# Optimization experiments

Hardware: AMD Instinct MI355X
Metric: run time of the kernel (lower is better)

The kernel has to match this reference:

```python
import jax, jax.numpy as jnp
import numpy as np

SCOPE = 63          # length of ricker inhibition filter (odd)
IN_CHANNELS = 256   # circulant matrix size == channel dim
SELF_CONNECT = False


def ricker(scope, width, damp, self_connect=False):
    # symmetric ricker (mexican-hat) wavelet of length `scope`, centered
    x = jnp.arange(scope, dtype=jnp.float32) - scope // 2
    w2 = width * width
    r = damp * (1.0 - x * x / w2) * jnp.exp(-x * x / (2.0 * w2))
    if not self_connect:
        r = r.at[scope // 2].set(0.0)  # no self-connection: zero center tap
    return r


def toeplitz1d_circular(f, size):
    # embed the centered length-`scope` filter into the first row of a
    # size x size circulant matrix (center tap on the diagonal, tails wrap)
    half = f.shape[0] // 2
    row0 = jnp.zeros(size, f.dtype)
    row0 = row0.at[: half + 1].set(f[half:])      # center + right tail
    row0 = row0.at[size - half:].set(f[:half])    # left tail wraps around
    idx = (jnp.arange(size)[:, None] - jnp.arange(size)[None, :]) % size
    return row0[idx]  # C[i, j] = row0[(i - j) mod size]


def setup_inputs() -> dict:
    key = jax.random.key(0)
    activations = jax.random.normal(key, (64, IN_CHANNELS, 56, 56), dtype=jnp.float32)
    damp = jnp.asarray(0.12, dtype=jnp.float32)   # learnable scalar
    width = jnp.asarray(3.0, dtype=jnp.float32)   # learnable scalar
    return {"activations": activations, "damp": damp, "width": width}


def reference(activations, damp, width):
    f = ricker(SCOPE, width, damp, SELF_CONNECT)
    tpl = toeplitz1d_circular(f, IN_CHANNELS)
    tpl_inv = jnp.linalg.inv(jnp.eye(IN_CHANNELS, dtype=f.dtype) - tpl)
    # apply inhibition matrix along the channel axis at every pixel
    return jnp.einsum('ij,bjhw->bihw', tpl_inv, activations)
```

## Files before the change

kernel.cpp:

```cpp
#include <hip/hip_runtime.h>


#define IN_CH 256
#define HW    3136
#define TP    64

typedef _Float16 f16x8  __attribute__((ext_vector_type(8)));
typedef float    f32x16 __attribute__((ext_vector_type(16)));


__global__ __launch_bounds__(256) void pi_build(const float* __restrict__ damp,
                                                const float* __restrict__ width,
                                                f16x8* __restrict__ afrag) {
    __shared__ float cS[256], gS[256], ctab[256], mS[256];
    int t = threadIdx.x;
    float w = width[0], dmp = damp[0];

    ctab[t] = cosf((float)t * 0.0245436926f );

    int x = (t < 128) ? t : t - 256;
    float cv = 0.0f;
    if (t != 0 && x >= -31 && x <= 31) {
        float fx2 = (float)(x * x);
        float w2  = w * w;
        cv = dmp * (1.0f - fx2 / w2) * expf(-fx2 / (2.0f * w2));
    }
    cS[t] = cv;
    __syncthreads();

    float lam = 0.0f;
#pragma unroll 8
    for (int n = 0; n < 256; n++) lam += cS[n] * ctab[(t * n) & 255];
    gS[t] = 1.0f / (1.0f - lam);
    __syncthreads();

    float md = 0.0f;
#pragma unroll 8
    for (int k = 0; k < 256; k++) md += gS[k] * ctab[(t * k) & 255];
    mS[t] = md * (1.0f / 256.0f);
    __syncthreads();

#pragma unroll
    for (int g = 0; g < 32; g++) {
        int gid = g * 256 + t;
        int l  = gid & 63;
        int tt = (gid >> 6) & 7;
        int s  = gid >> 9;
        int i     = 32 * tt + (l & 31);
        int kbase = 16 * s + 8 * (l >> 5);
        f16x8 h;
#pragma unroll
        for (int j = 0; j < 8; j++)
            h[j] = (_Float16)mS[(i - (kbase + j)) & 255];
        afrag[gid] = h;
    }
}

__device__ __forceinline__ void loads16(const float* __restrict__ src, float* v) {
#pragma unroll
    for (int j = 0; j < 8; j++) {
        v[j]     = src[(size_t)j * HW];
        v[8 + j] = src[(size_t)j * HW + 32];
    }
}

__device__ __forceinline__ void compute16(const float* v,
                                          const f16x8* __restrict__ afrag,
                                          int base, int lane,
                                          f32x16 acc[2][2]) {
    f16x8 b0, b1;
#pragma unroll
    for (int j = 0; j < 8; j++) {
        b0[j] = (_Float16)v[j];
        b1[j] = (_Float16)v[8 + j];
    }
    f16x8 a0 = afrag[(base + 0) * 64 + lane];
    f16x8 a1 = afrag[(base + 1) * 64 + lane];
    acc[0][0] = __builtin_amdgcn_mfma_f32_32x32x16_f16(a0, b0, acc[0][0], 0, 0, 0);
    acc[0][1] = __builtin_amdgcn_mfma_f32_32x32x16_f16(a0, b1, acc[0][1], 0, 0, 0);
    acc[1][0] = __builtin_amdgcn_mfma_f32_32x32x16_f16(a1, b0, acc[1][0], 0, 0, 0);
    acc[1][1] = __builtin_amdgcn_mfma_f32_32x32x16_f16(a1, b1, acc[1][1], 0, 0, 0);
}

__global__ __launch_bounds__(256, 4) void pi_gemm(const float* __restrict__ act,
                                                  float* __restrict__ out,
                                                  const f16x8* __restrict__ afrag) {
    int tid  = threadIdx.x;
    int lane = tid & 63;
    int wv   = tid >> 6;

    int b    = blockIdx.x / 49;
    int tile = blockIdx.x - b * 49;
    int p0   = tile * TP;

    int col   = lane & 31;
    int khalf = (lane >> 5) * 8;

    const float* actb = act + (size_t)b * (IN_CH * HW) + p0 + col;
    float*       outb = out + (size_t)b * (IN_CH * HW) + p0 + col;

    f32x16 acc[2][2] = {};

    float v0[16], v1[16];
    const float* ksrc = actb + (size_t)khalf * HW;

    loads16(ksrc, v0);
#pragma unroll
    for (int ss = 0; ss < 8; ss++) {
        loads16(ksrc + (size_t)(16 * (2 * ss + 1)) * HW, v1);
        compute16(v0, afrag, (2 * ss) * 8 + 2 * wv, lane, acc);
        if (ss < 7)
            loads16(ksrc + (size_t)(16 * (2 * ss + 2)) * HW, v0);
        compute16(v1, afrag, (2 * ss + 1) * 8 + 2 * wv, lane, acc);
    }

    int rb = 4 * (lane >> 5);
#pragma unroll
    for (int ti = 0; ti < 2; ti++) {
#pragma unroll
        for (int ni = 0; ni < 2; ni++) {
            float* dst = outb + (size_t)(64 * wv + 32 * ti + rb) * HW + 32 * ni;
#pragma unroll
            for (int r = 0; r < 16; r++) {
                int row = (r & 3) + 8 * (r >> 2);
                __builtin_nontemporal_store(acc[ti][ni][r], dst + (size_t)row * HW);
            }
        }
    }
}

extern "C" void kernel_launch(void* const* d_in, const int* in_sizes, int n_in,
                              void* d_out, int out_size, void* d_ws, size_t ws_size,
                              hipStream_t stream) {
    const float* act   = (const float*)d_in[0];
    const float* damp  = (const float*)d_in[1];
    const float* width = (const float*)d_in[2];
    float* out = (float*)d_out;

    f16x8* afrag = (f16x8*)d_ws;
    int batches = in_sizes[0] / (IN_CH * HW);

    pi_build<<<1, 256, 0, stream>>>(damp, width, afrag);
    pi_gemm<<<batches * 49, 256, 0, stream>>>(act, out, afrag);
}
```

Before: 383.3 us.

## Stage activation tiles through LDS with async global_load_lds pipeline

Replaces per-lane strided register loads of the activation tile with 16-byte global_load_lds transfers into a 4-deep LDS ring buffer, shared across the four waves. Each wave now loads only a quarter of the K slice and reads B fragments from LDS, with explicit vmcnt waits and barriers pipelining three stages ahead. This is meant to cut redundant global traffic, since each wave previously reloaded the full activation slice, and to widen the memory requests. In exchange it adds 32KB of LDS per block, which may limit occupancy at 4 blocks per CU, plus block-wide barriers.

```diff
diff --git a/kernel.cpp b/kernel.cpp
--- a/kernel.cpp
+++ b/kernel.cpp
@@ -4,9 +4,11 @@
 #define IN_CH 256
 #define HW    3136
 #define TP    64
+#define KS    32
 
 typedef _Float16 f16x8  __attribute__((ext_vector_type(8)));
 typedef float    f32x16 __attribute__((ext_vector_type(16)));
+typedef unsigned int u32;
 
 
 __global__ __launch_bounds__(256) void pi_build(const float* __restrict__ damp,
@@ -56,35 +58,17 @@
     }
 }
 
-__device__ __forceinline__ void loads16(const float* __restrict__ src, float* v) {
-#pragma unroll
-    for (int j = 0; j < 8; j++) {
-        v[j]     = src[(size_t)j * HW];
-        v[8 + j] = src[(size_t)j * HW + 32];
-    }
-}
-
-__device__ __forceinline__ void compute16(const float* v,
-                                          const f16x8* __restrict__ afrag,
-                                          int base, int lane,
-                                          f32x16 acc[2][2]) {
-    f16x8 b0, b1;
-#pragma unroll
-    for (int j = 0; j < 8; j++) {
-        b0[j] = (_Float16)v[j];
-        b1[j] = (_Float16)v[8 + j];
-    }
-    f16x8 a0 = afrag[(base + 0) * 64 + lane];
-    f16x8 a1 = afrag[(base + 1) * 64 + lane];
-    acc[0][0] = __builtin_amdgcn_mfma_f32_32x32x16_f16(a0, b0, acc[0][0], 0, 0, 0);
-    acc[0][1] = __builtin_amdgcn_mfma_f32_32x32x16_f16(a0, b1, acc[0][1], 0, 0, 0);
-    acc[1][0] = __builtin_amdgcn_mfma_f32_32x32x16_f16(a1, b0, acc[1][0], 0, 0, 0);
-    acc[1][1] = __builtin_amdgcn_mfma_f32_32x32x16_f16(a1, b1, acc[1][1], 0, 0, 0);
+__device__ __forceinline__ void gl_lds16(const float* g, const float* l) {
+    __builtin_amdgcn_global_load_lds(
+        (const __attribute__((address_space(1))) u32*)g,
+        (__attribute__((address_space(3))) u32*)l, 16, 0, 0);
 }
 
 __global__ __launch_bounds__(256, 4) void pi_gemm(const float* __restrict__ act,
                                                   float* __restrict__ out,
                                                   const f16x8* __restrict__ afrag) {
+    __shared__ float lds[4][KS][TP];
+
     int tid  = threadIdx.x;
     int lane = tid & 63;
     int wv   = tid >> 6;
@@ -93,33 +77,73 @@
     int tile = blockIdx.x - b * 49;
     int p0   = tile * TP;
 
-    int col   = lane & 31;
-    int khalf = (lane >> 5) * 8;
+    const float* actb = act + (size_t)b * (IN_CH * HW) + p0;
+    float*       outb = out + (size_t)b * (IN_CH * HW) + p0;
 
-    const float* actb = act + (size_t)b * (IN_CH * HW) + p0 + col;
-    float*       outb = out + (size_t)b * (IN_CH * HW) + p0 + col;
+    const float* gsrc = actb + (size_t)(lane >> 4) * HW + (lane & 15) * 4;
+
+    int lo = lane & 31;
+    int hi = lane >> 5;
 
     f32x16 acc[2][2] = {};
 
-    float v0[16], v1[16];
-    const float* ksrc = actb + (size_t)khalf * HW;
+#define STAGE(st) do {                                                         \
+    gl_lds16(gsrc + (size_t)((st) * KS + 8 * wv    ) * HW,                     \
+             &lds[(st) & 3][8 * wv    ][0]);                                   \
+    gl_lds16(gsrc + (size_t)((st) * KS + 8 * wv + 4) * HW,                     \
+             &lds[(st) & 3][8 * wv + 4][0]);                                   \
+} while (0)
 
-    loads16(ksrc, v0);
-#pragma unroll
-    for (int ss = 0; ss < 8; ss++) {
-        loads16(ksrc + (size_t)(16 * (2 * ss + 1)) * HW, v1);
-        compute16(v0, afrag, (2 * ss) * 8 + 2 * wv, lane, acc);
-        if (ss < 7)
-            loads16(ksrc + (size_t)(16 * (2 * ss + 2)) * HW, v0);
-        compute16(v1, afrag, (2 * ss + 1) * 8 + 2 * wv, lane, acc);
-    }
+#define WAITB(N) do {                                                          \
+    __builtin_amdgcn_sched_barrier(0);                                         \
+    asm volatile("s_waitcnt vmcnt(" #N ")" ::: "memory");                      \
+    __builtin_amdgcn_s_barrier();                                              \
+    __builtin_amdgcn_sched_barrier(0);                                         \
+} while (0)
 
-    int rb = 4 * (lane >> 5);
+#define KSTEP(t) do {                                                          \
+    const float (*buf)[TP] = lds[(t) & 3];                                     \
+    f16x8 bf0[2], bf1[2];                                                      \
+    _Pragma("unroll")                                                          \
+    for (int s = 0; s < 2; s++) {                                              \
+        _Pragma("unroll")                                                      \
+        for (int j = 0; j < 8; j++) {                                          \
+            bf0[s][j] = (_Float16)buf[16 * s + 8 * hi + j][lo];                \
+            bf1[s][j] = (_Float16)buf[16 * s + 8 * hi + j][32 + lo];           \
+        }                                                                      \
+    }                                                                          \
+    _Pragma("unroll")                                                          \
+    for (int s = 0; s < 2; s++) {                                              \
+        f16x8 a0 = afrag[((2 * (t) + s) * 8 + 2 * wv    ) * 64 + lane];        \
+        f16x8 a1 = afrag[((2 * (t) + s) * 8 + 2 * wv + 1) * 64 + lane];        \
+        acc[0][0] = __builtin_amdgcn_mfma_f32_32x32x16_f16(a0, bf0[s], acc[0][0], 0, 0, 0); \
+        acc[0][1] = __builtin_amdgcn_mfma_f32_32x32x16_f16(a0, bf1[s], acc[0][1], 0, 0, 0); \
+        acc[1][0] = __builtin_amdgcn_mfma_f32_32x32x16_f16(a1, bf0[s], acc[1][0], 0, 0, 0); \
+        acc[1][1] = __builtin_amdgcn_mfma_f32_32x32x16_f16(a1, bf1[s], acc[1][1], 0, 0, 0); \
+    }                                                                          \
+} while (0)
+
+    STAGE(0); STAGE(1); STAGE(2);
+
+    WAITB(4); STAGE(3); KSTEP(0);
+    WAITB(4); STAGE(4); KSTEP(1);
+    WAITB(4); STAGE(5); KSTEP(2);
+    WAITB(4); STAGE(6); KSTEP(3);
+    WAITB(4); STAGE(7); KSTEP(4);
+    WAITB(4);           KSTEP(5);
+    WAITB(2);           KSTEP(6);
+    WAITB(0);           KSTEP(7);
+
+#undef STAGE
+#undef WAITB
+#undef KSTEP
+
+    int rb = 4 * hi;
 #pragma unroll
     for (int ti = 0; ti < 2; ti++) {
 #pragma unroll
         for (int ni = 0; ni < 2; ni++) {
-            float* dst = outb + (size_t)(64 * wv + 32 * ti + rb) * HW + 32 * ni;
+            float* dst = outb + (size_t)(64 * wv + 32 * ti + rb) * HW + 32 * ni + lo;
 #pragma unroll
             for (int r = 0; r < 16; r++) {
                 int row = (r & 3) + 8 * (r >> 2);
```

New measurement: 364.5 us. 1.05x faster.
